# Kernel optimization log

Measured on AMD Instinct MI355X. Metric: run time of the kernel, lower is better.

The kernel has to match this reference:

```python
import jax, jax.numpy as jnp
import numpy as np

VAR_CXCY = 0.1   # variances[0]
VAR_WH = 0.2     # variances[1]
MIN_OVERLAP = 0.5
NEG_POS_RATIO = 3


def cxcy_to_xyxy(b):
    return jnp.concatenate([b[:, :2] - b[:, 2:] / 2, b[:, :2] + b[:, 2:] / 2], axis=-1)


def jaccard(a, b):
    # a: [O,4] xyxy, b: [P,4] xyxy -> [O,P]
    lt = jnp.maximum(a[:, None, :2], b[None, :, :2])
    rb = jnp.minimum(a[:, None, 2:], b[None, :, 2:])
    wh = jnp.clip(rb - lt, 0.0)
    inter = wh[..., 0] * wh[..., 1]
    area_a = (a[:, 2] - a[:, 0]) * (a[:, 3] - a[:, 1])
    area_b = (b[:, 2] - b[:, 0]) * (b[:, 3] - b[:, 1])
    return inter / (area_a[:, None] + area_b[None, :] - inter)


def xyxy_to_gcxgcy(boxes, priors):
    # boxes: [P,4] xyxy matched per-prior; priors: [P,4] cxcywh
    cxcy = (boxes[:, :2] + boxes[:, 2:]) / 2
    wh = boxes[:, 2:] - boxes[:, :2]
    g_cxcy = (cxcy - priors[:, :2]) / (priors[:, 2:] * VAR_CXCY)
    g_wh = jnp.log(wh / priors[:, 2:]) / VAR_WH
    return jnp.concatenate([g_cxcy, g_wh], axis=-1)


def _match_one(boxes, labels, priors, priors_xyxy):
    # boxes: [O,4] xyxy, labels: [O] int
    overlaps = jaccard(boxes, priors_xyxy)          # [O,P]
    prior_overlaps = overlaps.max(axis=0)            # [P]
    prior_objects = overlaps.argmax(axis=0)          # [P]
    object_priors = overlaps.argmax(axis=1)          # [O] best prior per object
    n_obj = boxes.shape[0]
    prior_objects = prior_objects.at[object_priors].set(jnp.arange(n_obj))
    prior_overlaps = prior_overlaps.at[object_priors].set(1.0)
    lab = labels[prior_objects]
    lab = jnp.where(prior_overlaps < MIN_OVERLAP, 0, lab)
    locs = xyxy_to_gcxgcy(boxes[prior_objects], priors)
    return locs, lab


def setup_inputs() -> dict:
    key = jax.random.key(0)
    B, P, C, O = 64, 8732, 81, 16
    ks = jax.random.split(key, 6)
    predict_locs = jax.random.normal(ks[0], (B, P, 4), dtype=jnp.float32)
    predict_confs = jax.random.normal(ks[1], (B, P, C), dtype=jnp.float32)
    # priors in cxcywh, valid sizes
    p_cxcy = jax.random.uniform(ks[2], (P, 2), minval=0.0, maxval=1.0)
    p_wh = jax.random.uniform(ks[2], (P, 2), minval=0.05, maxval=0.3)
    priors = jnp.concatenate([p_cxcy, p_wh], axis=-1).astype(jnp.float32)
    # targets: valid xyxy boxes in [0,1]
    t_cxcy = jax.random.uniform(ks[3], (B, O, 2), minval=0.2, maxval=0.8)
    t_wh = jax.random.uniform(ks[4], (B, O, 2), minval=0.05, maxval=0.4)
    target_boxes = jnp.concatenate([t_cxcy - t_wh / 2, t_cxcy + t_wh / 2], axis=-1).astype(jnp.float32)
    target_labels = jax.random.randint(ks[5], (B, O), 1, C)
    return {
        'predict_locs': predict_locs,
        'predict_confs': predict_confs,
        'target_boxes': target_boxes,
        'target_labels': target_labels,
        'priors': priors,
    }


def reference(predict_locs, predict_confs, target_boxes, target_labels, priors):
    priors_xyxy = cxcy_to_xyxy(priors)
    true_locs, true_confs = jax.vmap(
        lambda b, l: _match_one(b, l, priors, priors_xyxy)
    )(target_boxes, target_labels)              # [B,P,4], [B,P]

    pos = true_confs != 0                        # [B,P]
    n_pos = pos.sum(axis=1)                      # [B]
    n_pos_total = n_pos.sum().astype(predict_locs.dtype)

    # nn.L1Loss(reduction='mean') over the [n_pos_total, 4] gathered entries
    loc_loss = jnp.sum(jnp.abs(predict_locs - true_locs) * pos[..., None]) / (n_pos_total * 4)

    logp = jax.nn.log_softmax(predict_confs, axis=-1)
    ce = -jnp.take_along_axis(logp, true_confs[..., None], axis=-1)[..., 0]  # [B,P]

    ce_pos_sum = jnp.sum(jnp.where(pos, ce, 0.0))
    ce_neg = jnp.where(pos, 0.0, ce)
    # double-sort rank: rank of each prior when sorted by descending neg loss
    rank = jnp.argsort(jnp.argsort(-ce_neg, axis=1), axis=1)
    hard = rank < (NEG_POS_RATIO * n_pos)[:, None]
    ce_hard_sum = jnp.sum(jnp.where(hard, ce_neg, 0.0))

    conf_loss = (ce_hard_sum + ce_pos_sum) / n_pos_total
    return conf_loss + loc_loss
```

## Files before the change

### kernel.cpp

```cpp
#include <hip/hip_runtime.h>
#include <cstdint>
#include <cstddef>

constexpr int O_C   = 16;
constexpr int P_MAX = 8732;
constexpr int CH    = 4;
constexpr int CHP   = 2183;

__device__ __forceinline__ float waveSumF(float v) {
    #pragma unroll
    for (int off = 32; off; off >>= 1) v += __shfl_xor(v, off);
    return v;
}
__device__ __forceinline__ int waveSumI(int v) {
    #pragma unroll
    for (int off = 32; off; off >>= 1) v += __shfl_xor(v, off);
    return v;
}

__global__ __launch_bounds__(256) void matchA1(
    const float* __restrict__ target_boxes,
    const float* __restrict__ priors,
    float* __restrict__ ov_out,
    unsigned char* __restrict__ obj_out,
    unsigned long long* __restrict__ okey_part,
    int P)
{
    const int b    = blockIdx.x / CH;
    const int c    = blockIdx.x % CH;
    const int tid  = threadIdx.x;
    const int lane = tid & 63;
    const int wid  = tid >> 6;

    __shared__ float bx0[O_C], by0[O_C], bx1[O_C], by1[O_C], barea[O_C];
    __shared__ unsigned long long s_wb[O_C * 4];

    if (tid < O_C) {
        const float* tb = target_boxes + ((size_t)b * O_C + tid) * 4;
        float x0 = tb[0], y0 = tb[1], x1 = tb[2], y1 = tb[3];
        bx0[tid] = x0; by0[tid] = y0; bx1[tid] = x1; by1[tid] = y1;
        barea[tid] = (x1 - x0) * (y1 - y0);
    }
    __syncthreads();

    float bi[O_C]; int bp[O_C];
    #pragma unroll
    for (int o = 0; o < O_C; ++o) { bi[o] = -1.0f; bp[o] = 0; }

    const int p0 = c * CHP, p1 = min(p0 + CHP, P);
    for (int p = p0 + tid; p < p1; p += 256) {
        float4 pr = reinterpret_cast<const float4*>(priors)[p];
        float px0 = pr.x - pr.z * 0.5f, py0 = pr.y - pr.w * 0.5f;
        float px1 = pr.x + pr.z * 0.5f, py1 = pr.y + pr.w * 0.5f;
        float parea = (px1 - px0) * (py1 - py0);
        float bv = -1.0f; int bo = 0;
        #pragma unroll
        for (int o = 0; o < O_C; ++o) {
            float ix0 = fmaxf(px0, bx0[o]), iy0 = fmaxf(py0, by0[o]);
            float ix1 = fminf(px1, bx1[o]), iy1 = fminf(py1, by1[o]);
            float iw = fmaxf(ix1 - ix0, 0.0f), ih = fmaxf(iy1 - iy0, 0.0f);
            float inter = iw * ih;
            float iou = inter / (barea[o] + parea - inter);
            if (iou > bv) { bv = iou; bo = o; }
            if (iou > bi[o]) { bi[o] = iou; bp[o] = p; }
        }
        ov_out[(size_t)b * P + p]  = bv;
        obj_out[(size_t)b * P + p] = (unsigned char)bo;
    }

    #pragma unroll
    for (int o = 0; o < O_C; ++o) {
        unsigned long long k = (bi[o] >= 0.0f)
            ? (((unsigned long long)__float_as_uint(bi[o]) << 32) |
               (unsigned long long)(0xFFFFFFFFu - (unsigned)bp[o]))
            : 0ull;
        #pragma unroll
        for (int off = 32; off; off >>= 1) {
            unsigned long long k2 = __shfl_xor(k, off);
            if (k2 > k) k = k2;
        }
        if (lane == 0) s_wb[o * 4 + wid] = k;
    }
    __syncthreads();
    if (tid < O_C) {
        unsigned long long k = s_wb[tid * 4];
        #pragma unroll
        for (int w = 1; w < 4; ++w) if (s_wb[tid * 4 + w] > k) k = s_wb[tid * 4 + w];
        okey_part[(size_t)blockIdx.x * O_C + tid] = k;
    }
}

__global__ __launch_bounds__(256) void ce_stream(
    const float* __restrict__ confs,
    const float* __restrict__ ov_in,
    const unsigned char* __restrict__ obj_in,
    const unsigned long long* __restrict__ okey_part,
    const float* __restrict__ target_boxes,
    const int*   __restrict__ target_labels,
    const float* __restrict__ priors,
    const float* __restrict__ predict_locs,
    float* __restrict__ ce_out,
    float* __restrict__ loc_part,
    int P, int rows)
{
    const int tid  = threadIdx.x;
    const int lane = tid & 63;
    const int wid  = tid >> 6;
    const int row0 = blockIdx.x * 256;
    const int row  = row0 + tid;

    __shared__ float4 tbox[2][O_C];
    __shared__ int    tlab[2][O_C], topr[2][O_C];
    __shared__ float  s_facc[4];

    const int b0     = row0 / P;
    const int rsplit = min(row0 + 256, (b0 + 1) * P);
    const int b1     = (rsplit < row0 + 256) ? b0 + 1 : b0;

    if (tid < 2 * O_C) {
        const int seg = tid >> 4, o = tid & 15;
        const int bb  = seg ? b1 : b0;
        const float* tb = target_boxes + ((size_t)bb * O_C + o) * 4;
        tbox[seg][o] = make_float4(tb[0], tb[1], tb[2], tb[3]);
        tlab[seg][o] = target_labels[(size_t)bb * O_C + o];
        unsigned long long kk = 0ull;
        #pragma unroll
        for (int cc = 0; cc < CH; ++cc) {
            unsigned long long k2 = okey_part[((size_t)bb * CH + cc) * O_C + o];
            if (k2 > kk) kk = k2;
        }
        topr[seg][o] = (int)(0xFFFFFFFFu - (unsigned)(kk & 0xFFFFFFFFull));
    }
    __syncthreads();

    const int phase = row & 3;
    const float4* vp = reinterpret_cast<const float4*>(confs) + (((size_t)row * 81) >> 2);

    float mA = -3.0e38f, sA = 0.0f;
    float mB = -3.0e38f, sB = 0.0f;
    #pragma unroll
    for (int j = 0; j < 21; ++j) {
        float4 v = vp[j];
        const int eb = 4 * j - phase;
        float x0 = ((unsigned)(eb + 0) < 81u) ? v.x : -3.0e38f;
        float x1 = ((unsigned)(eb + 1) < 81u) ? v.y : -3.0e38f;
        float x2 = ((unsigned)(eb + 2) < 81u) ? v.z : -3.0e38f;
        float x3 = ((unsigned)(eb + 3) < 81u) ? v.w : -3.0e38f;
        float m4 = fmaxf(fmaxf(x0, x1), fmaxf(x2, x3));
        if (j & 1) {
            float mn = fmaxf(mB, m4);
            sB = sB * __expf(mB - mn)
               + __expf(x0 - mn) + __expf(x1 - mn)
               + __expf(x2 - mn) + __expf(x3 - mn);
            mB = mn;
        } else {
            float mn = fmaxf(mA, m4);
            sA = sA * __expf(mA - mn)
               + __expf(x0 - mn) + __expf(x1 - mn)
               + __expf(x2 - mn) + __expf(x3 - mn);
            mA = mn;
        }
    }
    float m = fmaxf(mA, mB);
    float s = sA * __expf(mA - m) + sB * __expf(mB - m);

    const int seg = (row >= rsplit) ? 1 : 0;
    const int bb  = seg ? b1 : b0;
    const int p   = row - bb * P;
    float ovv = ov_in[row];
    int   obj = obj_in[row];
    #pragma unroll
    for (int o = 0; o < O_C; ++o)
        if (topr[seg][o] == p) { obj = o; ovv = 1.0f; }
    const int l = (ovv < 0.5f) ? 0 : tlab[seg][obj];

    float xl  = confs[(size_t)row * 81 + l];
    float cev = m + __logf(s) - xl;
    ce_out[row] = l ? -cev : cev;

    float locacc = 0.0f;
    if (l) {
        float4 pr = reinterpret_cast<const float4*>(priors)[p];
        float4 tb = tbox[seg][obj];
        float cx = (tb.x + tb.z) * 0.5f, cy = (tb.y + tb.w) * 0.5f;
        float w  = tb.z - tb.x,          h  = tb.w - tb.y;
        float g0 = (cx - pr.x) / (pr.z * 0.1f);
        float g1 = (cy - pr.y) / (pr.w * 0.1f);
        float g2 = logf(w / pr.z) / 0.2f;
        float g3 = logf(h / pr.w) / 0.2f;
        float4 pl = reinterpret_cast<const float4*>(predict_locs)[row];
        locacc = fabsf(pl.x - g0) + fabsf(pl.y - g1) +
                 fabsf(pl.z - g2) + fabsf(pl.w - g3);
    }
    float a = waveSumF(locacc);
    if (lane == 0) s_facc[wid] = a;
    __syncthreads();
    if (tid == 0)
        loc_part[blockIdx.x] = s_facc[0] + s_facc[1] + s_facc[2] + s_facc[3];
}

__global__ __launch_bounds__(1024) void hard_kernel(
    const float* __restrict__ ce,
    int*   __restrict__ n_pos,
    float* __restrict__ ce_pos,
    float* __restrict__ ce_hard,
    int P)
{
    const int b    = blockIdx.x;
    const int tid  = threadIdx.x;
    const int lane = tid & 63;
    const int wid  = tid >> 6;

    __shared__ float s_v[P_MAX];
    __shared__ unsigned int hist[16][256];
    __shared__ unsigned int s_sel;
    __shared__ int s_kr;
    __shared__ float s_f[16], s_f2[16];
    __shared__ int s_i[16];

    const size_t base = (size_t)b * P;
    float possum = 0.0f, negsum = 0.0f;
    int cnt = 0;
    for (int p = tid; p < P; p += 1024) {
        float c = ce[base + p];
        unsigned u = __float_as_uint(c);
        float sv;
        if (u >> 31) { possum += -c; ++cnt; sv = 0.0f; }
        else         { negsum += c;         sv = c;    }
        s_v[p] = sv;
    }
    possum = waveSumF(possum);
    negsum = waveSumF(negsum);
    cnt    = waveSumI(cnt);
    if (lane == 0) { s_f[wid] = possum; s_f2[wid] = negsum; s_i[wid] = cnt; }
    __syncthreads();
    float negsum_t = 0.0f, possum_t = 0.0f; int np = 0;
    #pragma unroll
    for (int w = 0; w < 16; ++w) { negsum_t += s_f2[w]; possum_t += s_f[w]; np += s_i[w]; }
    if (tid == 0) { ce_pos[b] = possum_t; n_pos[b] = np; }

    const int K = 3 * np;
    if (K <= 0) { if (tid == 0) ce_hard[b] = 0.0f; return; }
    if (K >= P) { if (tid == 0) ce_hard[b] = negsum_t; return; }

    unsigned int prefix = 0; int kr = K;
    for (int shift = 24; shift >= 0; shift -= 8) {
        for (int i = tid; i < 16 * 256; i += 1024) (&hist[0][0])[i] = 0;
        __syncthreads();
        unsigned int maskHi = (shift == 24) ? 0u : (0xFFFFFFFFu << (shift + 8));
        for (int p = tid; p < P; p += 1024) {
            unsigned int u = __float_as_uint(s_v[p]);
            if ((u & maskHi) == prefix) atomicAdd(&hist[wid][(u >> shift) & 255], 1u);
        }
        __syncthreads();
        if (wid == 0) {
            unsigned h0 = 0, h1 = 0, h2 = 0, h3 = 0;
            #pragma unroll 4
            for (int w = 0; w < 16; ++w) {
                h0 += hist[w][lane * 4 + 0];
                h1 += hist[w][lane * 4 + 1];
                h2 += hist[w][lane * 4 + 2];
                h3 += hist[w][lane * 4 + 3];
            }
            unsigned own = h0 + h1 + h2 + h3;
            unsigned t = own;
            #pragma unroll
            for (int off = 1; off < 64; off <<= 1) {
                unsigned u = __shfl_down(t, off);
                if (lane + off >= 64) u = 0;
                t += u;
            }
            unsigned Tnext = t - own;
            unsigned cum3 = Tnext;
            unsigned cum2 = cum3 + h3;
            unsigned cum1 = cum2 + h2;
            unsigned cum0 = cum1 + h1;
            unsigned kru = (unsigned)kr;
            int selj = -1; unsigned cg = 0;
            if      (cum3 < kru && kru <= cum3 + h3) { selj = 3; cg = cum3; }
            else if (cum2 < kru && kru <= cum2 + h2) { selj = 2; cg = cum2; }
            else if (cum1 < kru && kru <= cum1 + h1) { selj = 1; cg = cum1; }
            else if (cum0 < kru && kru <= cum0 + h0) { selj = 0; cg = cum0; }
            if (selj >= 0) {
                s_sel = prefix | ((unsigned)(lane * 4 + selj) << shift);
                s_kr  = kr - (int)cg;
            }
        }
        __syncthreads();
        prefix = s_sel; kr = s_kr;
        __syncthreads();
    }

    float sumgt = 0.0f;
    for (int p = tid; p < P; p += 1024) {
        unsigned int u = __float_as_uint(s_v[p]);
        if (u > prefix) sumgt += s_v[p];
    }
    sumgt = waveSumF(sumgt);
    if (lane == 0) s_f[wid] = sumgt;
    __syncthreads();
    if (tid == 0) {
        float sg = 0.0f;
        #pragma unroll
        for (int w = 0; w < 16; ++w) sg += s_f[w];
        ce_hard[b] = sg + (float)kr * __uint_as_float(prefix);
    }
}

__global__ __launch_bounds__(256) void finalize_kernel(
    const int*   __restrict__ n_pos,
    const float* __restrict__ ce_pos,
    const float* __restrict__ ce_hard,
    const float* __restrict__ loc_part,
    float* __restrict__ out, int B, int nblk)
{
    __shared__ float s_f[4];
    __shared__ float s_res[3];
    const int tid  = threadIdx.x;
    const int lane = tid & 63;
    const int wid  = tid >> 6;

    float la = 0.0f;
    for (int i = tid; i < nblk; i += 256) la += loc_part[i];
    la = waveSumF(la);
    if (lane == 0) s_f[wid] = la;

    if (tid < 64) {
        int np = 0; float cp = 0.0f, ch = 0.0f;
        for (int b = lane; b < B; b += 64) {
            np += n_pos[b]; cp += ce_pos[b]; ch += ce_hard[b];
        }
        #pragma unroll
        for (int off = 32; off; off >>= 1) {
            np += __shfl_xor(np, off);
            cp += __shfl_xor(cp, off);
            ch += __shfl_xor(ch, off);
        }
        if (lane == 0) {
            s_res[0] = (float)np; s_res[1] = cp; s_res[2] = ch;
        }
    }
    __syncthreads();
    if (tid == 0) {
        float latot = s_f[0] + s_f[1] + s_f[2] + s_f[3];
        float npt = s_res[0];
        out[0] = (s_res[2] + s_res[1]) / npt + latot / (npt * 4.0f);
    }
}

extern "C" void kernel_launch(void* const* d_in, const int* in_sizes, int n_in,
                              void* d_out, int out_size, void* d_ws, size_t ws_size,
                              hipStream_t stream) {
    const float* predict_locs  = (const float*)d_in[0];
    const float* predict_confs = (const float*)d_in[1];
    const float* target_boxes  = (const float*)d_in[2];
    const int*   target_labels = (const int*)d_in[3];
    const float* priors        = (const float*)d_in[4];

    const int P = in_sizes[4] / 4;
    const int B = in_sizes[0] / (P * 4);
    const int rows = B * P;
    const int nblk = rows / 256;

    char* ws = (char*)d_ws;
    unsigned long long* okey_part = (unsigned long long*)ws;
    ws += (size_t)B * CH * O_C * sizeof(unsigned long long);
    float* ce      = (float*)ws; ws += (size_t)rows * sizeof(float);
    float* ov      = (float*)ws; ws += (size_t)rows * sizeof(float);
    float* loc_p   = (float*)ws; ws += (size_t)nblk * sizeof(float);
    int*   n_pos   = (int*)ws;   ws += (size_t)B * sizeof(int);
    float* ce_pos  = (float*)ws; ws += (size_t)B * sizeof(float);
    float* ce_hard = (float*)ws; ws += (size_t)B * sizeof(float);
    unsigned char* obj = (unsigned char*)ws; ws += (size_t)rows;

    matchA1<<<B * CH, 256, 0, stream>>>(target_boxes, priors, ov, obj, okey_part, P);
    ce_stream<<<nblk, 256, 0, stream>>>(predict_confs, ov, obj, okey_part,
                                        target_boxes, target_labels, priors,
                                        predict_locs, ce, loc_p, P, rows);
    hard_kernel<<<B, 1024, 0, stream>>>(ce, n_pos, ce_pos, ce_hard, P);
    finalize_kernel<<<1, 256, 0, stream>>>(n_pos, ce_pos, ce_hard, loc_p,
                                           (float*)d_out, B, rows / 256);
}
```

Baseline: 77.99 us.

## Recompute per-prior IoU argmax in CE kernel and fuse finalize into hard kernel

```diff
diff --git a/kernel.cpp b/kernel.cpp
--- a/kernel.cpp
+++ b/kernel.cpp
@@ -18,12 +18,11 @@
     return v;
 }
 
-__global__ __launch_bounds__(256) void matchA1(
+__global__ __launch_bounds__(256) void match_okey(
     const float* __restrict__ target_boxes,
     const float* __restrict__ priors,
-    float* __restrict__ ov_out,
-    unsigned char* __restrict__ obj_out,
     unsigned long long* __restrict__ okey_part,
+    int* __restrict__ counter,
     int P)
 {
     const int b    = blockIdx.x / CH;
@@ -32,6 +31,8 @@
     const int lane = tid & 63;
     const int wid  = tid >> 6;
 
+    if (blockIdx.x == 0 && tid == 0) *counter = 0;
+
     __shared__ float bx0[O_C], by0[O_C], bx1[O_C], by1[O_C], barea[O_C];
     __shared__ unsigned long long s_wb[O_C * 4];
 
@@ -53,7 +54,6 @@
         float px0 = pr.x - pr.z * 0.5f, py0 = pr.y - pr.w * 0.5f;
         float px1 = pr.x + pr.z * 0.5f, py1 = pr.y + pr.w * 0.5f;
         float parea = (px1 - px0) * (py1 - py0);
-        float bv = -1.0f; int bo = 0;
         #pragma unroll
         for (int o = 0; o < O_C; ++o) {
             float ix0 = fmaxf(px0, bx0[o]), iy0 = fmaxf(py0, by0[o]);
@@ -61,11 +61,8 @@
             float iw = fmaxf(ix1 - ix0, 0.0f), ih = fmaxf(iy1 - iy0, 0.0f);
             float inter = iw * ih;
             float iou = inter / (barea[o] + parea - inter);
-            if (iou > bv) { bv = iou; bo = o; }
             if (iou > bi[o]) { bi[o] = iou; bp[o] = p; }
         }
-        ov_out[(size_t)b * P + p]  = bv;
-        obj_out[(size_t)b * P + p] = (unsigned char)bo;
     }
 
     #pragma unroll
@@ -92,8 +89,6 @@
 
 __global__ __launch_bounds__(256) void ce_stream(
     const float* __restrict__ confs,
-    const float* __restrict__ ov_in,
-    const unsigned char* __restrict__ obj_in,
     const unsigned long long* __restrict__ okey_part,
     const float* __restrict__ target_boxes,
     const int*   __restrict__ target_labels,
@@ -110,6 +105,7 @@
     const int row  = row0 + tid;
 
     __shared__ float4 tbox[2][O_C];
+    __shared__ float  tarea[2][O_C];
     __shared__ int    tlab[2][O_C], topr[2][O_C];
     __shared__ float  s_facc[4];
 
@@ -121,8 +117,10 @@
         const int seg = tid >> 4, o = tid & 15;
         const int bb  = seg ? b1 : b0;
         const float* tb = target_boxes + ((size_t)bb * O_C + o) * 4;
-        tbox[seg][o] = make_float4(tb[0], tb[1], tb[2], tb[3]);
-        tlab[seg][o] = target_labels[(size_t)bb * O_C + o];
+        float x0 = tb[0], y0 = tb[1], x1 = tb[2], y1 = tb[3];
+        tbox[seg][o]  = make_float4(x0, y0, x1, y1);
+        tarea[seg][o] = (x1 - x0) * (y1 - y0);
+        tlab[seg][o]  = target_labels[(size_t)bb * O_C + o];
         unsigned long long kk = 0ull;
         #pragma unroll
         for (int cc = 0; cc < CH; ++cc) {
@@ -134,7 +132,8 @@
     __syncthreads();
 
     const int phase = row & 3;
-    const float4* vp = reinterpret_cast<const float4*>(confs) + (((size_t)row * 81) >> 2);
+    const float4* vp = reinterpret_cast<const float4*>(confs)
+                     + (((size_t)row * 81) >> 2);
 
     float mA = -3.0e38f, sA = 0.0f;
     float mB = -3.0e38f, sB = 0.0f;
@@ -167,8 +166,22 @@
     const int seg = (row >= rsplit) ? 1 : 0;
     const int bb  = seg ? b1 : b0;
     const int p   = row - bb * P;
-    float ovv = ov_in[row];
-    int   obj = obj_in[row];
+
+    float4 pr = reinterpret_cast<const float4*>(priors)[p];
+    float px0 = pr.x - pr.z * 0.5f, py0 = pr.y - pr.w * 0.5f;
+    float px1 = pr.x + pr.z * 0.5f, py1 = pr.y + pr.w * 0.5f;
+    float parea = (px1 - px0) * (py1 - py0);
+    float ovv = -1.0f; int obj = 0;
+    #pragma unroll
+    for (int o = 0; o < O_C; ++o) {
+        float4 tb = tbox[seg][o];
+        float ix0 = fmaxf(px0, tb.x), iy0 = fmaxf(py0, tb.y);
+        float ix1 = fminf(px1, tb.z), iy1 = fminf(py1, tb.w);
+        float iw = fmaxf(ix1 - ix0, 0.0f), ih = fmaxf(iy1 - iy0, 0.0f);
+        float inter = iw * ih;
+        float iou = inter / (tarea[seg][o] + parea - inter);
+        if (iou > ovv) { ovv = iou; obj = o; }
+    }
     #pragma unroll
     for (int o = 0; o < O_C; ++o)
         if (topr[seg][o] == p) { obj = o; ovv = 1.0f; }
@@ -180,7 +193,6 @@
 
     float locacc = 0.0f;
     if (l) {
-        float4 pr = reinterpret_cast<const float4*>(priors)[p];
         float4 tb = tbox[seg][obj];
         float cx = (tb.x + tb.z) * 0.5f, cy = (tb.y + tb.w) * 0.5f;
         float w  = tb.z - tb.x,          h  = tb.w - tb.y;
@@ -199,12 +211,15 @@
         loc_part[blockIdx.x] = s_facc[0] + s_facc[1] + s_facc[2] + s_facc[3];
 }
 
-__global__ __launch_bounds__(1024) void hard_kernel(
+__global__ __launch_bounds__(1024) void hard_finalize(
     const float* __restrict__ ce,
+    const float* __restrict__ loc_part,
     int*   __restrict__ n_pos,
     float* __restrict__ ce_pos,
     float* __restrict__ ce_hard,
-    int P)
+    int*   __restrict__ counter,
+    float* __restrict__ out,
+    int P, int B, int nblk)
 {
     const int b    = blockIdx.x;
     const int tid  = threadIdx.x;
@@ -214,7 +229,7 @@
     __shared__ float s_v[P_MAX];
     __shared__ unsigned int hist[16][256];
     __shared__ unsigned int s_sel;
-    __shared__ int s_kr;
+    __shared__ int s_kr, s_last;
     __shared__ float s_f[16], s_f2[16];
     __shared__ int s_i[16];
 
@@ -240,111 +255,105 @@
     if (tid == 0) { ce_pos[b] = possum_t; n_pos[b] = np; }
 
     const int K = 3 * np;
-    if (K <= 0) { if (tid == 0) ce_hard[b] = 0.0f; return; }
-    if (K >= P) { if (tid == 0) ce_hard[b] = negsum_t; return; }
-
-    unsigned int prefix = 0; int kr = K;
-    for (int shift = 24; shift >= 0; shift -= 8) {
-        for (int i = tid; i < 16 * 256; i += 1024) (&hist[0][0])[i] = 0;
-        __syncthreads();
-        unsigned int maskHi = (shift == 24) ? 0u : (0xFFFFFFFFu << (shift + 8));
+    if (K <= 0) {
+        if (tid == 0) ce_hard[b] = 0.0f;
+    } else if (K >= P) {
+        if (tid == 0) ce_hard[b] = negsum_t;
+    } else {
+        unsigned int prefix = 0; int kr = K;
+        for (int shift = 24; shift >= 0; shift -= 8) {
+            for (int i = tid; i < 16 * 256; i += 1024) (&hist[0][0])[i] = 0;
+            __syncthreads();
+            unsigned int maskHi = (shift == 24) ? 0u : (0xFFFFFFFFu << (shift + 8));
+            for (int p = tid; p < P; p += 1024) {
+                unsigned int u = __float_as_uint(s_v[p]);
+                if ((u & maskHi) == prefix) atomicAdd(&hist[wid][(u >> shift) & 255], 1u);
+            }
+            __syncthreads();
+            if (wid == 0) {
+                unsigned h0 = 0, h1 = 0, h2 = 0, h3 = 0;
+                #pragma unroll 4
+                for (int w = 0; w < 16; ++w) {
+                    h0 += hist[w][lane * 4 + 0];
+                    h1 += hist[w][lane * 4 + 1];
+                    h2 += hist[w][lane * 4 + 2];
+                    h3 += hist[w][lane * 4 + 3];
+                }
+                unsigned own = h0 + h1 + h2 + h3;
+                unsigned t = own;
+                #pragma unroll
+                for (int off = 1; off < 64; off <<= 1) {
+                    unsigned u = __shfl_down(t, off);
+                    if (lane + off >= 64) u = 0;
+                    t += u;
+                }
+                unsigned Tnext = t - own;
+                unsigned cum3 = Tnext;
+                unsigned cum2 = cum3 + h3;
+                unsigned cum1 = cum2 + h2;
+                unsigned cum0 = cum1 + h1;
+                unsigned kru = (unsigned)kr;
+                int selj = -1; unsigned cg = 0;
+                if      (cum3 < kru && kru <= cum3 + h3) { selj = 3; cg = cum3; }
+                else if (cum2 < kru && kru <= cum2 + h2) { selj = 2; cg = cum2; }
+                else if (cum1 < kru && kru <= cum1 + h1) { selj = 1; cg = cum1; }
+                else if (cum0 < kru && kru <= cum0 + h0) { selj = 0; cg = cum0; }
+                if (selj >= 0) {
+                    s_sel = prefix | ((unsigned)(lane * 4 + selj) << shift);
+                    s_kr  = kr - (int)cg;
+                }
+            }
+            __syncthreads();
+            prefix = s_sel; kr = s_kr;
+            __syncthreads();
+        }
+
+        float sumgt = 0.0f;
         for (int p = tid; p < P; p += 1024) {
             unsigned int u = __float_as_uint(s_v[p]);
-            if ((u & maskHi) == prefix) atomicAdd(&hist[wid][(u >> shift) & 255], 1u);
-        }
+            if (u > prefix) sumgt += s_v[p];
+        }
+        sumgt = waveSumF(sumgt);
+        if (lane == 0) s_f[wid] = sumgt;
         __syncthreads();
-        if (wid == 0) {
-            unsigned h0 = 0, h1 = 0, h2 = 0, h3 = 0;
-            #pragma unroll 4
-            for (int w = 0; w < 16; ++w) {
-                h0 += hist[w][lane * 4 + 0];
-                h1 += hist[w][lane * 4 + 1];
-                h2 += hist[w][lane * 4 + 2];
-                h3 += hist[w][lane * 4 + 3];
-            }
-            unsigned own = h0 + h1 + h2 + h3;
-            unsigned t = own;
+        if (tid == 0) {
+            float sg = 0.0f;
             #pragma unroll
-            for (int off = 1; off < 64; off <<= 1) {
-                unsigned u = __shfl_down(t, off);
-                if (lane + off >= 64) u = 0;
-                t += u;
-            }
-            unsigned Tnext = t - own;
-            unsigned cum3 = Tnext;
-            unsigned cum2 = cum3 + h3;
-            unsigned cum1 = cum2 + h2;
-            unsigned cum0 = cum1 + h1;
-            unsigned kru = (unsigned)kr;
-            int selj = -1; unsigned cg = 0;
-            if      (cum3 < kru && kru <= cum3 + h3) { selj = 3; cg = cum3; }
-            else if (cum2 < kru && kru <= cum2 + h2) { selj = 2; cg = cum2; }
-            else if (cum1 < kru && kru <= cum1 + h1) { selj = 1; cg = cum1; }
-            else if (cum0 < kru && kru <= cum0 + h0) { selj = 0; cg = cum0; }
-            if (selj >= 0) {
-                s_sel = prefix | ((unsigned)(lane * 4 + selj) << shift);
-                s_kr  = kr - (int)cg;
-            }
-        }
+            for (int w = 0; w < 16; ++w) sg += s_f[w];
+            ce_hard[b] = sg + (float)kr * __uint_as_float(prefix);
+        }
+    }
+
+    __threadfence();
+    __syncthreads();
+    if (tid == 0) s_last = (atomicAdd(counter, 1) == B - 1) ? 1 : 0;
+    __syncthreads();
+    if (s_last) {
+        __threadfence();
+        float la = 0.0f;
+        for (int i = tid; i < nblk; i += 1024) la += loc_part[i];
+        la = waveSumF(la);
+        if (lane == 0) s_f[wid] = la;
         __syncthreads();
-        prefix = s_sel; kr = s_kr;
-        __syncthreads();
-    }
-
-    float sumgt = 0.0f;
-    for (int p = tid; p < P; p += 1024) {
-        unsigned int u = __float_as_uint(s_v[p]);
-        if (u > prefix) sumgt += s_v[p];
-    }
-    sumgt = waveSumF(sumgt);
-    if (lane == 0) s_f[wid] = sumgt;
-    __syncthreads();
-    if (tid == 0) {
-        float sg = 0.0f;
-        #pragma unroll
-        for (int w = 0; w < 16; ++w) sg += s_f[w];
-        ce_hard[b] = sg + (float)kr * __uint_as_float(prefix);
-    }
-}
-
-__global__ __launch_bounds__(256) void finalize_kernel(
-    const int*   __restrict__ n_pos,
-    const float* __restrict__ ce_pos,
-    const float* __restrict__ ce_hard,
-    const float* __restrict__ loc_part,
-    float* __restrict__ out, int B, int nblk)
-{
-    __shared__ float s_f[4];
-    __shared__ float s_res[3];
-    const int tid  = threadIdx.x;
-    const int lane = tid & 63;
-    const int wid  = tid >> 6;
-
-    float la = 0.0f;
-    for (int i = tid; i < nblk; i += 256) la += loc_part[i];
-    la = waveSumF(la);
-    if (lane == 0) s_f[wid] = la;
-
-    if (tid < 64) {
-        int np = 0; float cp = 0.0f, ch = 0.0f;
-        for (int b = lane; b < B; b += 64) {
-            np += n_pos[b]; cp += ce_pos[b]; ch += ce_hard[b];
-        }
-        #pragma unroll
-        for (int off = 32; off; off >>= 1) {
-            np += __shfl_xor(np, off);
-            cp += __shfl_xor(cp, off);
-            ch += __shfl_xor(ch, off);
-        }
-        if (lane == 0) {
-            s_res[0] = (float)np; s_res[1] = cp; s_res[2] = ch;
-        }
-    }
-    __syncthreads();
-    if (tid == 0) {
-        float latot = s_f[0] + s_f[1] + s_f[2] + s_f[3];
-        float npt = s_res[0];
-        out[0] = (s_res[2] + s_res[1]) / npt + latot / (npt * 4.0f);
+        if (tid < 64) {
+            int npT = 0; float cp = 0.0f, chd = 0.0f;
+            for (int bb = tid; bb < B; bb += 64) {
+                npT += n_pos[bb]; cp += ce_pos[bb]; chd += ce_hard[bb];
+            }
+            #pragma unroll
+            for (int off = 32; off; off >>= 1) {
+                npT += __shfl_xor(npT, off);
+                cp  += __shfl_xor(cp, off);
+                chd += __shfl_xor(chd, off);
+            }
+            if (tid == 0) {
+                float latot = 0.0f;
+                #pragma unroll
+                for (int w = 0; w < 16; ++w) latot += s_f[w];
+                float npt = (float)npT;
+                out[0] = (chd + cp) / npt + latot / (npt * 4.0f);
+            }
+        }
     }
 }
 
@@ -360,24 +369,24 @@
     const int P = in_sizes[4] / 4;
     const int B = in_sizes[0] / (P * 4);
     const int rows = B * P;
+    const int nmatch = B * CH;
     const int nblk = rows / 256;
 
     char* ws = (char*)d_ws;
     unsigned long long* okey_part = (unsigned long long*)ws;
-    ws += (size_t)B * CH * O_C * sizeof(unsigned long long);
+    ws += (size_t)nmatch * O_C * sizeof(unsigned long long);
     float* ce      = (float*)ws; ws += (size_t)rows * sizeof(float);
-    float* ov      = (float*)ws; ws += (size_t)rows * sizeof(float);
     float* loc_p   = (float*)ws; ws += (size_t)nblk * sizeof(float);
     int*   n_pos   = (int*)ws;   ws += (size_t)B * sizeof(int);
     float* ce_pos  = (float*)ws; ws += (size_t)B * sizeof(float);
     float* ce_hard = (float*)ws; ws += (size_t)B * sizeof(float);
-    unsigned char* obj = (unsigned char*)ws; ws += (size_t)rows;
-
-    matchA1<<<B * CH, 256, 0, stream>>>(target_boxes, priors, ov, obj, okey_part, P);
-    ce_stream<<<nblk, 256, 0, stream>>>(predict_confs, ov, obj, okey_part,
+    int*   counter = (int*)ws;   ws += sizeof(int);
+
+    match_okey<<<nmatch, 256, 0, stream>>>(target_boxes, priors, okey_part,
+                                           counter, P);
+    ce_stream<<<nblk, 256, 0, stream>>>(predict_confs, okey_part,
                                         target_boxes, target_labels, priors,
                                         predict_locs, ce, loc_p, P, rows);
-    hard_kernel<<<B, 1024, 0, stream>>>(ce, n_pos, ce_pos, ce_hard, P);
-    finalize_kernel<<<1, 256, 0, stream>>>(n_pos, ce_pos, ce_hard, loc_p,
-                                           (float*)d_out, B, rows / 256);
-}
+    hard_finalize<<<B, 1024, 0, stream>>>(ce, loc_p, n_pos, ce_pos, ce_hard,
+                                          counter, (float*)d_out, P, B, nblk);
+}
```

Result: slower. 100.2 us (+28.5%).
